# Performance work log

Hardware: AMD Instinct MI355X
Metric: run time of the kernel (lower is better)

Reference implementation:

```python
import jax, jax.numpy as jnp
import numpy as np

NT = 100000   # total word nodes (B graphs * N nodes)
B = 50        # number of graphs in the batch
E = 1600000   # total edges
V = 15000     # vocab (num_word)
D_IN = 128    # h_inp
D_H = 128     # h_dim


def setup_inputs() -> dict:
    key = jax.random.key(0)
    ks = jax.random.split(key, 12)
    return {
        "node_ids": jax.random.randint(ks[0], (NT,), 0, V),
        "src": jax.random.randint(ks[1], (E,), 0, NT),
        "dst": jax.random.randint(ks[2], (E,), 0, NT),
        "edge_weight": jax.random.uniform(ks[3], (E,), dtype=jnp.float32),
        "y_data": jax.random.uniform(ks[4], (B,), dtype=jnp.float32),
        "word_embeds": jax.random.normal(ks[5], (V, D_IN), dtype=jnp.float32) * 0.1,
        "W1": jax.random.normal(ks[6], (D_IN, D_H), dtype=jnp.float32) * 0.05,
        "b1": jax.random.normal(ks[7], (D_H,), dtype=jnp.float32) * 0.05,
        "W2": jax.random.normal(ks[8], (D_H, D_H), dtype=jnp.float32) * 0.05,
        "b2": jax.random.normal(ks[9], (D_H,), dtype=jnp.float32) * 0.05,
        "W_out": jax.random.normal(ks[10], (D_H, 1), dtype=jnp.float32) * 0.05,
        "b_out": jax.random.normal(ks[11], (1,), dtype=jnp.float32) * 0.05,
    }


def _word_graph_layer(h, W, b, src, dst, edge_weight, deg):
    # Linear projection, then DGL u_mul_e + mean aggregation over incoming edges.
    Wh = h @ W + b                                   # [NT, D]
    m = Wh[src] * edge_weight[:, None]               # gather + edge-weight mul, [E, D]
    s = jax.ops.segment_sum(m, dst, num_segments=NT)  # scatter-add, [NT, D]
    # mean over incoming messages; nodes with no in-edges keep 0 (DGL semantics)
    return jnp.where(deg[:, None] > 0, s / jnp.maximum(deg, 1.0)[:, None], 0.0)


def reference(node_ids, src, dst, edge_weight, y_data, word_embeds,
              W1, b1, W2, b2, W_out, b_out):
    deg = jax.ops.segment_sum(jnp.ones_like(edge_weight), dst, num_segments=NT)
    h = word_embeds[node_ids]                        # [NT, D_IN]
    h = _word_graph_layer(h, W1, b1, src, dst, edge_weight, deg)
    h = jax.nn.leaky_relu(h, negative_slope=0.01)
    h = _word_graph_layer(h, W2, b2, src, dst, edge_weight, deg)
    # per-graph mean pool; equal graph sizes so padded mean == true mean
    word_pool = h.reshape(B, NT // B, D_H).mean(axis=1)   # [B, D_H]
    logits = (word_pool @ W_out + b_out).reshape(-1)      # [B]
    # binary_cross_entropy_with_logits, mean reduction (numerically stable)
    loss = jnp.mean(jnp.maximum(logits, 0.0) - logits * y_data
                    + jnp.log1p(jnp.exp(-jnp.abs(logits))))
    y_pred = jax.nn.sigmoid(logits)[:, None]              # [B, 1]
    return (loss, y_pred)
```

## Files before the change

kernel.cpp:

```cpp
#include <hip/hip_runtime.h>
#include <hip/hip_fp16.h>
#include <math.h>

#define NT 100000
#define B_GRAPHS 50
#define NE 1600000
#define V 15000
#define D 128
#define NODES_PER_GRAPH (NT / B_GRAPHS)

#define POOL_N (B_GRAPHS * D + B_GRAPHS)

#define BSH 8
#define BIN_DSTS 256
#define NBIN ((NT + BIN_DSTS - 1) / BIN_DSTS)
#define SLACK (3 * BIN_DSTS)
#define EPB 4096
#define NFB ((NE + EPB - 1) / EPB)
#define BUF_SORT 5632
#define STAGE_STRIDE 4608
#define PAY_STRIDE (STAGE_STRIDE + SLACK)
#define PAY_TAIL 512
#define PR 16
#define PROJ_BLOCKS ((V + PR - 1) / PR)

__device__ __forceinline__ unsigned enc2_e5m2(float a, float b) {
  unsigned ha = __half_as_ushort(__float2half(a));
  unsigned hb = __half_as_ushort(__float2half(b));
  ha = ((ha + 0x7fu + ((ha >> 8) & 1u)) >> 8) & 0xffu;
  hb = ((hb + 0x7fu + ((hb >> 8) & 1u)) >> 8) & 0xffu;
  return ha | (hb << 8);
}
__device__ __forceinline__ unsigned enc4_e5m2(float a, float b, float c, float d) {
  return enc2_e5m2(a, b) | (enc2_e5m2(c, d) << 16);
}

__global__ __launch_bounds__(512)
void k_pb(const float* __restrict__ embeds, const float* __restrict__ W1,
          const float* __restrict__ b1, unsigned* __restrict__ P1p8,
          float* __restrict__ pool, int2* __restrict__ payTail,
          const int* __restrict__ src, const int* __restrict__ dst,
          const float* __restrict__ ew, const int* __restrict__ node_ids,
          int* __restrict__ binCursor, int2* __restrict__ stage) {
  __shared__ union {
    struct {
      int h[512], sc[512], gbase[512], cur[512];
      int wsum[8], woff[8];
      unsigned short binOf[EPB];
      int2 buf[EPB];
    } f;
    struct {
      float sE[PR][D];
      float sO[PR][D];
    } p;
  } U;
  int t = threadIdx.x;
  if (blockIdx.x < NFB) {
    int lane = t & 63, wv = t >> 6;
    U.f.h[t] = 0;
    __syncthreads();
    int base = blockIdx.x * EPB;
    int d_[EPB / 512], b_[EPB / 512];
#pragma unroll
    for (int i = 0; i < EPB / 512; ++i) {
      int e = base + i * 512 + t;
      int d = (e < NE) ? dst[e] : -1;
      d_[i] = d;
      b_[i] = (d >= 0) ? (d >> BSH) : -1;
      if (d >= 0) atomicAdd(&U.f.h[b_[i]], 1);
    }
    __syncthreads();
    int c = U.f.h[t];
    int v = c;
#pragma unroll
    for (int off = 1; off < 64; off <<= 1) {
      int x = __shfl_up(v, off);
      if (lane >= off) v += x;
    }
    if (lane == 63) U.f.wsum[wv] = v;
    __syncthreads();
    if (t == 0) {
      int a = 0;
#pragma unroll
      for (int i = 0; i < 8; ++i) { U.f.woff[i] = a; a += U.f.wsum[i]; }
    }
    __syncthreads();
    int incl = v + U.f.woff[wv];
    U.f.sc[t] = incl;
    U.f.cur[t] = incl - c;
    if (t < NBIN && c > 0) U.f.gbase[t] = atomicAdd(&binCursor[t], c);
    __syncthreads();
    int total = U.f.sc[511];
#pragma unroll
    for (int i = 0; i < EPB / 512; ++i) {
      int e = base + i * 512 + t;
      if (e < NE) {
        int s = src[e];
        unsigned uw = __float_as_uint(ew[e]);
        unsigned wb = (uw + 0x7fffu + ((uw >> 16) & 1u)) & 0xffff0000u;
        int wid = node_ids[s];
        int dl = d_[i] & (BIN_DSTS - 1);
        int p = atomicAdd(&U.f.cur[b_[i]], 1);
        U.f.buf[p] = make_int2((int)(wb | (unsigned)wid), s | (dl << 17));
        U.f.binOf[p] = (unsigned short)b_[i];
      }
    }
    __syncthreads();
    for (int i = t; i < total; i += 512) {
      int b = U.f.binOf[i];
      int local = i - (U.f.sc[b] - U.f.h[b]);
      stage[(size_t)b * STAGE_STRIDE + U.f.gbase[b] + local] = U.f.buf[i];
    }
  } else {
    int pb = blockIdx.x - NFB;
    if (pb == 0) {
      for (int i = t; i < POOL_N; i += 512) pool[i] = 0.f;
      for (int i = t; i < PAY_TAIL; i += 512) payTail[i] = make_int2(0, 0);
    }
    int row0 = pb * PR;
    for (int i = t; i < PR * D; i += 512) {
      int r = i >> 7, c = i & 127;
      int vv = row0 + r;
      U.p.sE[r][c] = (vv < V) ? embeds[(size_t)vv * D + c] : 0.f;
    }
    __syncthreads();
    int c = t & 127, rg = (t >> 7) * 4;
    float bd = b1[c];
    float acc[4];
#pragma unroll
    for (int r = 0; r < 4; ++r) acc[r] = bd;
#pragma unroll 4
    for (int k = 0; k < D; ++k) {
      float w = W1[k * D + c];
#pragma unroll
      for (int r = 0; r < 4; ++r) acc[r] = fmaf(U.p.sE[rg + r][k], w, acc[r]);
    }
#pragma unroll
    for (int r = 0; r < 4; ++r) U.p.sO[rg + r][c] = acc[r];
    __syncthreads();
    {
      int r = t >> 5, li = t & 31;
      int vv = row0 + r;
      if (vv < V)
        P1p8[(size_t)vv * 32 + li] =
            enc4_e5m2(U.p.sO[r][4 * li], U.p.sO[r][4 * li + 1],
                      U.p.sO[r][4 * li + 2], U.p.sO[r][4 * li + 3]);
    }
  }
}

__global__ __launch_bounds__(512)
void k_binsort(const int2* __restrict__ stage, const int* __restrict__ binCnt,
               int* __restrict__ rowD, int* __restrict__ cntD,
               int2* __restrict__ pay) {
  __shared__ int h2[BIN_DSTS], cur2[BIN_DSTS];
  __shared__ float invD[BIN_DSTS];
  __shared__ int wsum4[4], woff4[4];
  __shared__ int sh_end;
  __shared__ int2 buf[BUF_SORT];
  int b = blockIdx.x, t = threadIdx.x;
  int lane = t & 63, wv = t >> 6;
  int cnt = binCnt[b];
  int sb = b * STAGE_STRIDE;
  int pb = b * PAY_STRIDE;
  int dst0 = b << BSH;
  if (t < BIN_DSTS) h2[t] = 0;
  __syncthreads();
  for (int i = t; i < cnt; i += 512)
    atomicAdd(&h2[(stage[sb + i].y >> 17) & 255], 1);
  __syncthreads();
  int c = (t < BIN_DSTS) ? h2[t] : 0;
  int pc = (c + 3) & ~3;
  int v = (t < BIN_DSTS) ? pc : 0;
#pragma unroll
  for (int off = 1; off < 64; off <<= 1) {
    int x = __shfl_up(v, off);
    if (lane >= off) v += x;
  }
  if (lane == 63 && wv < 4) wsum4[wv] = v;
  __syncthreads();
  if (t == 0) {
    int a = 0;
#pragma unroll
    for (int i = 0; i < 4; ++i) { woff4[i] = a; a += wsum4[i]; }
    sh_end = a;
  }
  __syncthreads();
  if (t < BIN_DSTS) {
    int myoff = v + woff4[wv] - pc;
    invD[t] = (c > 0) ? (1.0f / (float)c) : 0.0f;
    cur2[t] = myoff;
    int n = dst0 + t;
    if (n < NT) { rowD[n] = pb + myoff; cntD[n] = c; }
  }
  __syncthreads();
  int end = sh_end + 24;
  if (end > PAY_STRIDE) end = PAY_STRIDE;
  for (int i = t; i < end; i += 512) buf[i] = make_int2(0, 0);
  __syncthreads();
  for (int i = t; i < cnt; i += 512) {
    int2 r = stage[sb + i];
    int dl = (r.y >> 17) & 255;
    float w = __uint_as_float((unsigned)r.x & 0xffff0000u);
    float wp = w * invD[dl];
    unsigned wh = (unsigned)__half_as_ushort(__float2half(wp));
    int p = atomicAdd(&cur2[dl], 1);
    buf[p] = make_int2((int)((wh << 16) | ((unsigned)r.x & 0xffffu)), r.y & 0x1ffff);
  }
  __syncthreads();
  for (int i = t; i < end; i += 512) pay[pb + i] = buf[i];
}

template<bool USE_WID>
__device__ __forceinline__ int pick_idx(const int4& q, int half) {
  int lo = USE_WID ? (q.x & 0xffff) : q.y;
  int hi = USE_WID ? (q.z & 0xffff) : q.w;
  return half ? hi : lo;
}
__device__ __forceinline__ void consume2h(const int4& q, unsigned v, int half,
                                          __half2& A01, __half2& A23, __half2& SW) {
  unsigned wm = (unsigned)(half ? q.z : q.x);
  unsigned wd = (wm >> 16) | (wm & 0xffff0000u);
  unsigned hp0 = ((v & 0xffu) << 8) | ((v & 0xff00u) << 16);
  unsigned hp1 = ((v >> 8) & 0xff00u) | (v & 0xff000000u);
  __half2 w2 = *(__half2*)&wd;
  A01 = __hfma2(w2, *(__half2*)&hp0, A01);
  A23 = __hfma2(w2, *(__half2*)&hp1, A23);
  SW = __hadd2(SW, w2);
}

template<bool USE_WID>
__device__ __forceinline__ void gather_row(const int2* __restrict__ pay,
                                           const unsigned* __restrict__ tab,
                                           int beg, int cnt, int li, int half,
                                           __half2& A01, __half2& A23, __half2& SW) {
  int G = (cnt + 3) >> 2;
  const int4* __restrict__ pp = (const int4*)(pay + beg);
  int4 q0a = pp[0], q0b = pp[1];
  int4 q1a = pp[2], q1b = pp[3];
  int4 q2a = pp[4], q2b = pp[5];
  int4 q3a = pp[6], q3b = pp[7];
  int4 q4a = pp[8], q4b = pp[9];
  unsigned va0 = tab[(size_t)pick_idx<USE_WID>(q0a, half) * 32 + li];
  unsigned vb0 = tab[(size_t)pick_idx<USE_WID>(q0b, half) * 32 + li];
  unsigned va1 = tab[(size_t)pick_idx<USE_WID>(q1a, half) * 32 + li];
  unsigned vb1 = tab[(size_t)pick_idx<USE_WID>(q1b, half) * 32 + li];
  unsigned va2 = tab[(size_t)pick_idx<USE_WID>(q2a, half) * 32 + li];
  unsigned vb2 = tab[(size_t)pick_idx<USE_WID>(q2b, half) * 32 + li];
  for (int g = 0; g < G; ++g) {
    unsigned vn0 = tab[(size_t)pick_idx<USE_WID>(q3a, half) * 32 + li];
    unsigned vn1 = tab[(size_t)pick_idx<USE_WID>(q3b, half) * 32 + li];
    int4 qna = pp[2 * g + 10];
    int4 qnb = pp[2 * g + 11];
    consume2h(q0a, va0, half, A01, A23, SW);
    consume2h(q0b, vb0, half, A01, A23, SW);
    q0a = q1a; q0b = q1b; q1a = q2a; q1b = q2b; q2a = q3a; q2b = q3b;
    q3a = q4a; q3b = q4b; q4a = qna; q4b = qnb;
    va0 = va1; vb0 = vb1; va1 = va2; vb1 = vb2; va2 = vn0; vb2 = vn1;
  }
}

#define NPW1 10
__global__ void k_agg1(const int2* __restrict__ pay,
                       const int* __restrict__ rowD, const int* __restrict__ cntD,
                       const unsigned* __restrict__ P1p8,
                       unsigned* __restrict__ h1p8) {
  int w = threadIdx.x >> 6, lane = threadIdx.x & 63;
  int li = lane & 31, half = lane >> 5;
  int nbase = blockIdx.x * (4 * NPW1) + w * NPW1;
  for (int i = 0; i < NPW1; ++i) {
    int n = nbase + i;
    int beg = __builtin_amdgcn_readfirstlane(rowD[n]);
    int cnt = __builtin_amdgcn_readfirstlane(cntD[n]);
    __half2 A01 = __half2half2(__float2half(0.f));
    __half2 A23 = A01, SW = A01;
    gather_row<true>(pay, P1p8, beg, cnt, li, half, A01, A23, SW);
    float2 f01 = __half22float2(A01);
    float2 f23 = __half22float2(A23);
    float a0 = f01.x, a1 = f01.y, a2 = f23.x, a3 = f23.y;
    a0 += __shfl_down(a0, 32);
    a1 += __shfl_down(a1, 32);
    a2 += __shfl_down(a2, 32);
    a3 += __shfl_down(a3, 32);
    if (lane < 32) {
      float x0 = a0, x1 = a1, x2 = a2, x3 = a3;
      x0 = (x0 > 0.f) ? x0 : 0.01f * x0;
      x1 = (x1 > 0.f) ? x1 : 0.01f * x1;
      x2 = (x2 > 0.f) ? x2 : 0.01f * x2;
      x3 = (x3 > 0.f) ? x3 : 0.01f * x3;
      h1p8[(size_t)n * 32 + li] = enc4_e5m2(x0, x1, x2, x3);
    }
  }
}

#define NPW2 10
#define BLKS_PER_G (NODES_PER_GRAPH / (4 * NPW2))
__global__ void k_agg2(const int2* __restrict__ pay,
                       const int* __restrict__ rowD, const int* __restrict__ cntD,
                       const unsigned* __restrict__ h1p8,
                       float* __restrict__ pool) {
  int g = blockIdx.x / BLKS_PER_G;
  int chunk = blockIdx.x % BLKS_PER_G;
  int w = threadIdx.x >> 6, lane = threadIdx.x & 63;
  int li = lane & 31, half = lane >> 5;
  int nbase = g * NODES_PER_GRAPH + chunk * (4 * NPW2) + w * NPW2;
  __half2 A01 = __half2half2(__float2half(0.f));
  __half2 A23 = A01, SW = A01;
  for (int i = 0; i < NPW2; ++i) {
    int n = nbase + i;
    int beg = __builtin_amdgcn_readfirstlane(rowD[n]);
    int cnt = __builtin_amdgcn_readfirstlane(cntD[n]);
    gather_row<false>(pay, h1p8, beg, cnt, li, half, A01, A23, SW);
  }
  float2 f01 = __half22float2(A01);
  float2 f23 = __half22float2(A23);
  float s0 = f01.x, s1 = f01.y, s2 = f23.x, s3 = f23.y;
  float sc = __low2float(SW);
  s0 += __shfl_down(s0, 32);
  s1 += __shfl_down(s1, 32);
  s2 += __shfl_down(s2, 32);
  s3 += __shfl_down(s3, 32);
  sc += __shfl_down(sc, 32);
  __shared__ float sS[4 * 128];
  __shared__ float sC[4];
  if (lane < 32) {
    sS[w * 128 + 4 * li + 0] = s0;
    sS[w * 128 + 4 * li + 1] = s1;
    sS[w * 128 + 4 * li + 2] = s2;
    sS[w * 128 + 4 * li + 3] = s3;
  }
  if (lane == 0) sC[w] = sc;
  __syncthreads();
  int t = threadIdx.x;
  if (t < 128) {
    float v = sS[t] + sS[128 + t] + sS[256 + t] + sS[384 + t];
    atomicAdd(&pool[g * D + t], v);
  }
  if (t == 0) atomicAdd(&pool[B_GRAPHS * D + g], sC[0] + sC[1] + sC[2] + sC[3]);
}

__global__ void k_final(const float* __restrict__ poolS, const float* __restrict__ poolC,
                        const float* __restrict__ W2, const float* __restrict__ b2,
                        const float* __restrict__ W_out, const float* __restrict__ b_out,
                        const float* __restrict__ y, float* __restrict__ out) {
  __shared__ float w2o[D];
  __shared__ float s2oArr[D];
  __shared__ float s2o_sh;
  __shared__ float logits[64];
  int t = threadIdx.x;
  int w = t >> 6, lane = t & 63;
  if (t < D) {
    float acc = 0.f;
    for (int d = 0; d < D; ++d) acc = fmaf(W2[t * D + d], W_out[d], acc);
    w2o[t] = acc;
  } else {
    int j = t - D;
    s2oArr[j] = b2[j] * W_out[j];
  }
  __syncthreads();
  if (t < 64) {
    float v = s2oArr[lane] + s2oArr[64 + lane];
#pragma unroll
    for (int off = 32; off > 0; off >>= 1) v += __shfl_down(v, off);
    if (lane == 0) s2o_sh = v;
  }
  __syncthreads();
  float s2o = s2o_sh;
  float bout = b_out[0];
  const float invN = 1.0f / (float)NODES_PER_GRAPH;
  for (int g = w; g < B_GRAPHS; g += 4) {
    float v = poolS[g * D + lane] * w2o[lane]
            + poolS[g * D + 64 + lane] * w2o[64 + lane];
#pragma unroll
    for (int off = 32; off > 0; off >>= 1) v += __shfl_down(v, off);
    if (lane == 0) {
      float l = v * invN + poolC[g] * invN * s2o + bout;
      logits[g] = l;
      out[1 + g] = 1.0f / (1.0f + expf(-l));
    }
  }
  __syncthreads();
  if (t < 64) {
    float term = 0.f;
    if (lane < B_GRAPHS) {
      float l = logits[lane];
      term = fmaxf(l, 0.f) - l * y[lane] + log1pf(expf(-fabsf(l)));
    }
#pragma unroll
    for (int off = 32; off > 0; off >>= 1) term += __shfl_down(term, off);
    if (lane == 0) out[0] = term / (float)B_GRAPHS;
  }
}

extern "C" void kernel_launch(void* const* d_in, const int* in_sizes, int n_in,
                              void* d_out, int out_size, void* d_ws, size_t ws_size,
                              hipStream_t stream) {
  const int*   node_ids = (const int*)d_in[0];
  const int*   src      = (const int*)d_in[1];
  const int*   dst      = (const int*)d_in[2];
  const float* ew       = (const float*)d_in[3];
  const float* y        = (const float*)d_in[4];
  const float* embeds   = (const float*)d_in[5];
  const float* W1       = (const float*)d_in[6];
  const float* b1       = (const float*)d_in[7];
  const float* W2       = (const float*)d_in[8];
  const float* b2       = (const float*)d_in[9];
  const float* W_out    = (const float*)d_in[10];
  const float* b_out    = (const float*)d_in[11];
  float* out = (float*)d_out;
  (void)in_sizes; (void)n_in; (void)out_size; (void)ws_size;

  char* ws = (char*)d_ws;
  size_t off = 0;
  auto alloc = [&](size_t bytes) {
    size_t r = off;
    off = (off + bytes + 511) & ~(size_t)511;
    return r;
  };
  size_t o_binCur = alloc(512 * 4);
  size_t o_pool   = alloc((size_t)POOL_N * 4);
  size_t o_rowD   = alloc((size_t)(NT + 1) * 4);
  size_t o_cntD   = alloc((size_t)NT * 4);
  size_t o_P1p8   = alloc((size_t)V * 32 * 4);
  size_t o_h1p8   = alloc((size_t)NT * 32 * 4);
  size_t o_stage  = alloc((size_t)NBIN * STAGE_STRIDE * 8);
  size_t o_pay    = alloc(((size_t)NBIN * PAY_STRIDE + PAY_TAIL) * 8);

  int*      binCursor= (int*)(ws + o_binCur);
  float*    pool     = (float*)(ws + o_pool);
  int*      rowD     = (int*)(ws + o_rowD);
  int*      cntD     = (int*)(ws + o_cntD);
  unsigned* P1p8     = (unsigned*)(ws + o_P1p8);
  unsigned* h1p8     = (unsigned*)(ws + o_h1p8);
  int2*     stage    = (int2*)(ws + o_stage);
  int2*     pay      = (int2*)(ws + o_pay);
  int2*     payTail  = pay + (size_t)NBIN * PAY_STRIDE;

  hipMemsetAsync(binCursor, 0, 512 * 4, stream);
  k_pb<<<NFB + PROJ_BLOCKS, 512, 0, stream>>>(embeds, W1, b1, P1p8, pool, payTail,
                                              src, dst, ew, node_ids, binCursor, stage);
  k_binsort<<<NBIN, 512, 0, stream>>>(stage, binCursor, rowD, cntD, pay);
  k_agg1<<<NT / (4 * NPW1), 256, 0, stream>>>(pay, rowD, cntD, P1p8, h1p8);
  k_agg2<<<B_GRAPHS * BLKS_PER_G, 256, 0, stream>>>(pay, rowD, cntD, h1p8, pool);
  k_final<<<1, 256, 0, stream>>>(pool, pool + B_GRAPHS * D, W2, b2, W_out, b_out, y, out);
}
```

Before: 251.4 us.

## Replace layer-2 edge gather with per-source graph-weight matrix pooled as dense matmul

Because only the per-graph mean pool of layer 2 is needed, the second aggregation is rewritten algebraically: during binsort each edge's normalized weight is atomically accumulated into a per-source, per-graph half-precision coefficient matrix. A new dense kernel then multiplies h1 by this matrix using fdot2, writes per-block partials, and a reduce kernel sums them. This replaces the irregular second edge gather with streaming reads, at the cost of many half2 atomics in binsort, an extra zeroed 12.8MB buffer, and fp16 accumulation precision in the coefficients.

New measurement: 343.7 us. +36.7%, slower.

```diff
diff --git a/kernel.cpp b/kernel.cpp
--- a/kernel.cpp
+++ b/kernel.cpp
@@ -24,6 +24,21 @@
 #define PR 16
 #define PROJ_BLOCKS ((V + PR - 1) / PR)
 
+#define KPH (NT / 2)
+#define GPAD 64
+#define CMAT_U (KPH * GPAD)
+#define POOL_BLKS 250
+#define KP_CHUNK (KPH / POOL_BLKS)
+#define POOL_ITERS (KP_CHUNK / 4)
+
+typedef _Float16 half2_t __attribute__((ext_vector_type(2)));
+
+#if defined(__has_builtin)
+#if __has_builtin(__builtin_amdgcn_fdot2)
+#define HAVE_FDOT2 1
+#endif
+#endif
+
 __device__ __forceinline__ unsigned enc2_e5m2(float a, float b) {
   unsigned ha = __half_as_ushort(__float2half(a));
   unsigned hb = __half_as_ushort(__float2half(b));
@@ -41,7 +56,8 @@
           float* __restrict__ pool, int2* __restrict__ payTail,
           const int* __restrict__ src, const int* __restrict__ dst,
           const float* __restrict__ ew, const int* __restrict__ node_ids,
-          int* __restrict__ binCursor, int2* __restrict__ stage) {
+          int* __restrict__ binCursor, int2* __restrict__ stage,
+          unsigned* __restrict__ Cmat) {
   __shared__ union {
     struct {
       int h[512], sc[512], gbase[512], cur[512];
@@ -117,6 +133,12 @@
       for (int i = t; i < POOL_N; i += 512) pool[i] = 0.f;
       for (int i = t; i < PAY_TAIL; i += 512) payTail[i] = make_int2(0, 0);
     }
+    {
+      int4* cm4 = (int4*)Cmat;
+      const int CM4 = CMAT_U / 4;
+      for (int i = pb * 512 + t; i < CM4; i += PROJ_BLOCKS * 512)
+        cm4[i] = make_int4(0, 0, 0, 0);
+    }
     int row0 = pb * PR;
     for (int i = t; i < PR * D; i += 512) {
       int r = i >> 7, c = i & 127;
@@ -152,7 +174,8 @@
 __global__ __launch_bounds__(512)
 void k_binsort(const int2* __restrict__ stage, const int* __restrict__ binCnt,
                int* __restrict__ rowD, int* __restrict__ cntD,
-               int2* __restrict__ pay) {
+               int2* __restrict__ pay, unsigned* __restrict__ Cmat,
+               float* __restrict__ poolC) {
   __shared__ int h2[BIN_DSTS], cur2[BIN_DSTS];
   __shared__ float invD[BIN_DSTS];
   __shared__ int wsum4[4], woff4[4];
@@ -164,6 +187,12 @@
   int sb = b * STAGE_STRIDE;
   int pb = b * PAY_STRIDE;
   int dst0 = b << BSH;
+  int g0 = dst0 / NODES_PER_GRAPH;
+  int bnd = (g0 + 1) * NODES_PER_GRAPH - dst0;
+  int gg1 = g0 + 1; if (gg1 > B_GRAPHS - 1) gg1 = B_GRAPHS - 1;
+  int col0 = (g0 < 25) ? g0 : g0 + 7;
+  int col1 = (gg1 < 25) ? gg1 : gg1 + 7;
+  float sg0 = 0.f, sg1 = 0.f;
   if (t < BIN_DSTS) h2[t] = 0;
   __syncthreads();
   for (int i = t; i < cnt; i += 512)
@@ -206,9 +235,25 @@
     unsigned wh = (unsigned)__half_as_ushort(__float2half(wp));
     int p = atomicAdd(&cur2[dl], 1);
     buf[p] = make_int2((int)((wh << 16) | ((unsigned)r.x & 0xffffu)), r.y & 0x1ffff);
+    int srcn = r.y & 0x1ffff;
+    int hi = (dl >= bnd) ? 1 : 0;
+    unsigned av = wh << (16 * (srcn & 1));
+    int col = hi ? col1 : col0;
+    __half2 hv = __builtin_bit_cast(__half2, av);
+    unsafeAtomicAdd((__half2*)(Cmat + ((size_t)(srcn >> 1) * GPAD + col)), hv);
+    if (hi) sg1 += wp; else sg0 += wp;
   }
   __syncthreads();
   for (int i = t; i < end; i += 512) pay[pb + i] = buf[i];
+#pragma unroll
+  for (int off = 32; off > 0; off >>= 1) {
+    sg0 += __shfl_down(sg0, off);
+    sg1 += __shfl_down(sg1, off);
+  }
+  if (lane == 0) {
+    if (sg0 != 0.f) atomicAdd(&poolC[g0], sg0);
+    if (sg1 != 0.f) atomicAdd(&poolC[gg1], sg1);
+  }
 }
 
 template<bool USE_WID>
@@ -293,50 +338,69 @@
   }
 }
 
-#define NPW2 10
-#define BLKS_PER_G (NODES_PER_GRAPH / (4 * NPW2))
-__global__ void k_agg2(const int2* __restrict__ pay,
-                       const int* __restrict__ rowD, const int* __restrict__ cntD,
-                       const unsigned* __restrict__ h1p8,
-                       float* __restrict__ pool) {
-  int g = blockIdx.x / BLKS_PER_G;
-  int chunk = blockIdx.x % BLKS_PER_G;
-  int w = threadIdx.x >> 6, lane = threadIdx.x & 63;
-  int li = lane & 31, half = lane >> 5;
-  int nbase = g * NODES_PER_GRAPH + chunk * (4 * NPW2) + w * NPW2;
-  __half2 A01 = __half2half2(__float2half(0.f));
-  __half2 A23 = A01, SW = A01;
-  for (int i = 0; i < NPW2; ++i) {
-    int n = nbase + i;
-    int beg = __builtin_amdgcn_readfirstlane(rowD[n]);
-    int cnt = __builtin_amdgcn_readfirstlane(cntD[n]);
-    gather_row<false>(pay, h1p8, beg, cnt, li, half, A01, A23, SW);
-  }
-  float2 f01 = __half22float2(A01);
-  float2 f23 = __half22float2(A23);
-  float s0 = f01.x, s1 = f01.y, s2 = f23.x, s3 = f23.y;
-  float sc = __low2float(SW);
-  s0 += __shfl_down(s0, 32);
-  s1 += __shfl_down(s1, 32);
-  s2 += __shfl_down(s2, 32);
-  s3 += __shfl_down(s3, 32);
-  sc += __shfl_down(sc, 32);
-  __shared__ float sS[4 * 128];
-  __shared__ float sC[4];
-  if (lane < 32) {
-    sS[w * 128 + 4 * li + 0] = s0;
-    sS[w * 128 + 4 * li + 1] = s1;
-    sS[w * 128 + 4 * li + 2] = s2;
-    sS[w * 128 + 4 * li + 3] = s3;
-  }
-  if (lane == 0) sC[w] = sc;
-  __syncthreads();
+__global__ __launch_bounds__(1024)
+void k_pool(const unsigned* __restrict__ h1p8, const unsigned* __restrict__ Cmat,
+            float* __restrict__ part) {
+  __shared__ float lacc[B_GRAPHS * D];
   int t = threadIdx.x;
-  if (t < 128) {
-    float v = sS[t] + sS[128 + t] + sS[256 + t] + sS[384 + t];
-    atomicAdd(&pool[g * D + t], v);
-  }
-  if (t == 0) atomicAdd(&pool[B_GRAPHS * D + g], sC[0] + sC[1] + sC[2] + sC[3]);
+  for (int i = t; i < B_GRAPHS * D; i += 1024) lacc[i] = 0.f;
+  __syncthreads();
+  int d = t & 127;
+  int ghu = __builtin_amdgcn_readfirstlane((t >> 7) & 1);
+  int ksu = __builtin_amdgcn_readfirstlane(t >> 8);
+  int kp0 = blockIdx.x * KP_CHUNK + ksu;
+  const unsigned* __restrict__ hp = h1p8 + ((size_t)(2 * kp0) * 32 + (d >> 2));
+  const unsigned* __restrict__ cp = Cmat + ((size_t)kp0 * GPAD + ghu * 32);
+  int sh = 8 * (d & 3);
+  float acc[25];
+#pragma unroll
+  for (int j = 0; j < 25; ++j) acc[j] = 0.f;
+  for (int i = 0; i < POOL_ITERS; ++i) {
+    unsigned v0 = hp[0], v1 = hp[32];
+    hp += 256;
+    unsigned pk = (((v0 >> sh) & 0xffu) << 8) | (((v1 >> sh) & 0xffu) << 24);
+#ifdef HAVE_FDOT2
+    half2_t h2 = __builtin_bit_cast(half2_t, pk);
+#pragma unroll
+    for (int j = 0; j < 25; ++j) {
+      half2_t c2 = __builtin_bit_cast(half2_t, cp[j]);
+      acc[j] = __builtin_amdgcn_fdot2(h2, c2, acc[j], false);
+    }
+#else
+    float h0f = __half2float(__ushort_as_half((unsigned short)(pk & 0xffffu)));
+    float h1f = __half2float(__ushort_as_half((unsigned short)(pk >> 16)));
+#pragma unroll
+    for (int j = 0; j < 25; ++j) {
+      unsigned cw = cp[j];
+      acc[j] = fmaf(h0f, __half2float(__ushort_as_half((unsigned short)(cw & 0xffffu))), acc[j]);
+      acc[j] = fmaf(h1f, __half2float(__ushort_as_half((unsigned short)(cw >> 16))), acc[j]);
+    }
+#endif
+    cp += 256;
+  }
+#pragma unroll
+  for (int j = 0; j < 25; ++j) {
+    int g = ghu * 25 + j;
+    atomicAdd(&lacc[g * D + d], acc[j]);
+  }
+  __syncthreads();
+  float* pb = part + (size_t)blockIdx.x * (B_GRAPHS * D);
+  for (int i = t; i < B_GRAPHS * D; i += 1024) pb[i] = lacc[i];
+}
+
+__global__ __launch_bounds__(256)
+void k_reduce(const float* __restrict__ part, float* __restrict__ pool) {
+  __shared__ float red[3][64];
+  int t = threadIdx.x;
+  int c = blockIdx.x * 64 + (t & 63);
+  int q = t >> 6;
+  int p0 = (q * POOL_BLKS) >> 2, p1 = ((q + 1) * POOL_BLKS) >> 2;
+  float s = 0.f;
+#pragma unroll 8
+  for (int p = p0; p < p1; ++p) s += part[(size_t)p * (B_GRAPHS * D) + c];
+  if (q) red[q - 1][t & 63] = s;
+  __syncthreads();
+  if (!q) pool[c] = s + red[0][t & 63] + red[1][t & 63] + red[2][t & 63];
 }
 
 __global__ void k_final(const float* __restrict__ poolS, const float* __restrict__ poolC,
@@ -425,6 +489,7 @@
   size_t o_h1p8   = alloc((size_t)NT * 32 * 4);
   size_t o_stage  = alloc((size_t)NBIN * STAGE_STRIDE * 8);
   size_t o_pay    = alloc(((size_t)NBIN * PAY_STRIDE + PAY_TAIL) * 8);
+  size_t o_Cmat   = alloc((size_t)CMAT_U * 4);
 
   int*      binCursor= (int*)(ws + o_binCur);
   float*    pool     = (float*)(ws + o_pool);
@@ -434,13 +499,18 @@
   unsigned* h1p8     = (unsigned*)(ws + o_h1p8);
   int2*     stage    = (int2*)(ws + o_stage);
   int2*     pay      = (int2*)(ws + o_pay);
+  unsigned* Cmat     = (unsigned*)(ws + o_Cmat);
   int2*     payTail  = pay + (size_t)NBIN * PAY_STRIDE;
-
-  hipMemsetAsync(binCursor, 0, 512 * 4, stream);
+  float*    part     = (float*)(ws + o_stage);
+
+  (void)hipMemsetAsync(binCursor, 0, 512 * 4, stream);
   k_pb<<<NFB + PROJ_BLOCKS, 512, 0, stream>>>(embeds, W1, b1, P1p8, pool, payTail,
-                                              src, dst, ew, node_ids, binCursor, stage);
-  k_binsort<<<NBIN, 512, 0, stream>>>(stage, binCursor, rowD, cntD, pay);
+                                              src, dst, ew, node_ids, binCursor, stage,
+                                              Cmat);
+  k_binsort<<<NBIN, 512, 0, stream>>>(stage, binCursor, rowD, cntD, pay, Cmat,
+                                      pool + B_GRAPHS * D);
   k_agg1<<<NT / (4 * NPW1), 256, 0, stream>>>(pay, rowD, cntD, P1p8, h1p8);
-  k_agg2<<<B_GRAPHS * BLKS_PER_G, 256, 0, stream>>>(pay, rowD, cntD, h1p8, pool);
+  k_pool<<<POOL_BLKS, 1024, 0, stream>>>(h1p8, Cmat, part);
+  k_reduce<<<B_GRAPHS * D / 64, 256, 0, stream>>>(part, pool);
   k_final<<<1, 256, 0, stream>>>(pool, pool + B_GRAPHS * D, W2, b2, W_out, b_out, y, out);
 }
```
